# Performance work log

Measured on AMD Instinct MI355X. Metric: run time of the kernel, lower is better.

The kernel has to match this reference:

```python
import jax, jax.numpy as jnp
import numpy as np

EPS = 1e-12  # F.normalize default eps

def _l2norm(a, axis):
    n = jnp.sqrt(jnp.sum(a * a, axis=axis, keepdims=True))
    return a / jnp.maximum(n, EPS)

def setup_inputs() -> dict:
    key = jax.random.key(0)
    kx, kc = jax.random.split(key)
    x = jax.random.normal(kx, (32, 64, 64, 64), dtype=jnp.float32)        # [B,C,H,W]
    codebook = 0.2 * jax.random.normal(kc, (512, 64), dtype=jnp.float32)  # nn.init.normal_(w, 0, 0.2)
    return {"x": x, "codebook": codebook}

def reference(x, codebook):
    # mode == 'angular': normalize codebook rows and x along dim=1 (channels)
    cb = _l2norm(codebook, axis=1)          # [K,C]
    xn = _l2norm(x, axis=1)                 # [B,C,H,W]
    # x.transpose(-1, dim) with dim=1 -> swap axes 1 and 3
    xt = jnp.swapaxes(xn, 1, -1)            # [B,W,H,C]
    B, W, H, C = xt.shape
    flat = xt.reshape(-1, C)                # [N,C]
    d = (jnp.sum(cb * cb, axis=1)[None, :]
         + jnp.sum(flat * flat, axis=1, keepdims=True)
         - 2.0 * flat @ cb.T)               # [N,K]
    idx = jnp.argmin(d, axis=1)             # [N]
    codes = cb[idx].reshape(B, W, H, C)
    indices = idx.reshape(B, W, H)
    codes = jnp.swapaxes(codes, 1, -1)      # back to [B,C,H,W]
    indices = jnp.swapaxes(indices, 1, -1)  # [B,H,W]
    return codes, indices
```

## Files before the change

### kernel.cpp

```cpp
#include <hip/hip_runtime.h>

#define VQ_EPS    1e-12f
#define VQ_WINDOW 0.01f
#define VQ_CAP    12

typedef short bf16x8 __attribute__((ext_vector_type(8)));
typedef float f32x4  __attribute__((ext_vector_type(4)));

static __device__ __forceinline__ unsigned short f2bf(float f) {
    unsigned u = __float_as_uint(f);
    u += 0x7fffu + ((u >> 16) & 1u);
    return (unsigned short)(u >> 16);
}

static __device__ __forceinline__ unsigned f2ord(float f) {
    unsigned b = __float_as_uint(f);
    return (b & 0x80000000u) ? ~b : (b | 0x80000000u);
}

static __device__ __forceinline__ void wave_lds_fence() {
    asm volatile("s_waitcnt lgkmcnt(0)" ::: "memory");
}

__global__ __launch_bounds__(64) void cb_prep_kernel(const float* __restrict__ cb,
                                                     float* __restrict__ cbn,
                                                     unsigned short* __restrict__ cbB,
                                                     float* __restrict__ kn2,
                                                     float* __restrict__ kn2p) {
    const int k = blockIdx.x;
    const int c = threadIdx.x;
    float v = cb[k * 64 + c];
    float s = v * v;
    #pragma unroll
    for (int off = 32; off > 0; off >>= 1) s += __shfl_xor(s, off, 64);
    float n = sqrtf(s);
    float cn = v / fmaxf(n, VQ_EPS);
    cbn[k * 64 + c] = cn;

    const int ntile = k >> 4, col = k & 15;
    const int ks = c >> 5, quad = (c >> 3) & 3, j = c & 7;
    cbB[(((ntile * 2 + ks) * 64) + quad * 16 + col) * 8 + j] = f2bf(cn);

    float s2 = cn * cn;
    #pragma unroll
    for (int off = 32; off > 0; off >>= 1) s2 += __shfl_xor(s2, off, 64);
    if (c == 0) { kn2[k] = s2; kn2p[k] = s2 + 2.0f; }
}

__global__ __launch_bounds__(1024, 8) void vq_mfma_kernel(const float* __restrict__ x,
                                                      const float* __restrict__ cbn,
                                                      const unsigned short* __restrict__ cbB,
                                                      const float* __restrict__ kn2,
                                                      const float* __restrict__ kn2p,
                                                      float* __restrict__ codes,
                                                      float* __restrict__ idxout) {
    __shared__ __align__(16) unsigned short lcb[32768];
    __shared__ unsigned long long spack[256];
    __shared__ int slist[256][VQ_CAP];
    __shared__ int scnt[256];

    const int t    = threadIdx.x;
    const int lane = t & 63;
    const int wid  = t >> 6;
    const int col  = lane & 15;
    const int quad = lane >> 4;
    const int wr   = wid & 3;
    const int rsel = wid >> 2;
    const int wpix = wr * 16 + col;
    const int pbase = rsel * 64;
    const int pslot = pbase + wpix;

    const int rowid = blockIdx.x * 4 + rsel;
    const int b = rowid >> 6;
    const int h = rowid & 63;
    const float* xblk = x + ((size_t)b << 18) + (h << 6);

    if (quad == 0) { scnt[pslot] = 0; spack[pslot] = 0xFFFFFFFFFFFFFFFFull; }

    float xv[16];
    #pragma unroll
    for (int ks = 0; ks < 2; ++ks)
        #pragma unroll
        for (int j = 0; j < 8; ++j)
            xv[ks * 8 + j] = xblk[(size_t)(ks * 32 + quad * 8 + j) * 4096 + wpix];

    {
        const uint4* g4 = (const uint4*)cbB;
        uint4*       l4 = (uint4*)lcb;
        #pragma unroll
        for (int r = 0; r < 4; ++r) l4[r * 1024 + t] = g4[r * 1024 + t];
    }

    float ssp = 0.0f;
    #pragma unroll
    for (int i = 0; i < 16; ++i) ssp = fmaf(xv[i], xv[i], ssp);
    ssp += __shfl_xor(ssp, 16);
    ssp += __shfl_xor(ssp, 32);
    const float m2a = -2.0f * (1.0f / fmaxf(sqrtf(ssp), VQ_EPS));
    float m2r[4];
    #pragma unroll
    for (int r = 0; r < 4; ++r) m2r[r] = __shfl(m2a, quad * 4 + r);
    const float m2P = __shfl(m2a, lane >> 2);

    bf16x8 afrag[2];
    #pragma unroll
    for (int ks = 0; ks < 2; ++ks)
        #pragma unroll
        for (int j = 0; j < 8; ++j)
            ((unsigned short*)&afrag[ks])[j] = f2bf(xv[ks * 8 + j]);

    __syncthreads();

    const bf16x8* lBf = (const bf16x8*)lcb;

    unsigned run1[4] = {0xFFFFFFFFu, 0xFFFFFFFFu, 0xFFFFFFFFu, 0xFFFFFFFFu};
    unsigned run2[4] = {0xFFFFFFFFu, 0xFFFFFFFFu, 0xFFFFFFFFu, 0xFFFFFFFFu};
    #pragma unroll 4
    for (int nt = 0; nt < 32; ++nt) {
        bf16x8 b0 = lBf[(nt * 2 + 0) * 64 + lane];
        bf16x8 b1 = lBf[(nt * 2 + 1) * 64 + lane];
        f32x4 c = {0.0f, 0.0f, 0.0f, 0.0f};
        c = __builtin_amdgcn_mfma_f32_16x16x32_bf16(afrag[0], b0, c, 0, 0, 0);
        c = __builtin_amdgcn_mfma_f32_16x16x32_bf16(afrag[1], b1, c, 0, 0, 0);
        const float    kn   = kn2p[nt * 16 + col];
        const unsigned kidx = (unsigned)(nt * 16 + col);
        #pragma unroll
        for (int r = 0; r < 4; ++r) {
            float s = fmaf(m2r[r], c[r], kn);
            unsigned key = (__float_as_uint(s) & 0xFFFFFE00u) | kidx;
            unsigned mx  = max(run1[r], key);
            run1[r] = min(run1[r], key);
            run2[r] = min(run2[r], mx);
        }
    }

    float thr[4];
    #pragma unroll
    for (int r = 0; r < 4; ++r) {
        unsigned v = run1[r];
        v = min(v, (unsigned)__shfl_xor((int)v, 1));
        v = min(v, (unsigned)__shfl_xor((int)v, 2));
        v = min(v, (unsigned)__shfl_xor((int)v, 4));
        v = min(v, (unsigned)__shfl_xor((int)v, 8));
        thr[r] = __uint_as_float(v & 0xFFFFFE00u) + VQ_WINDOW;
    }

    bool f = false;
    #pragma unroll
    for (int r = 0; r < 4; ++r)
        f |= (__uint_as_float(run2[r] & 0xFFFFFE00u) <= thr[r]);
    const unsigned long long waveflag = __ballot(f);

    if (waveflag != 0ull) {
        #pragma unroll 4
        for (int nt = 0; nt < 32; ++nt) {
            bf16x8 b0 = lBf[(nt * 2 + 0) * 64 + lane];
            bf16x8 b1 = lBf[(nt * 2 + 1) * 64 + lane];
            f32x4 c = {0.0f, 0.0f, 0.0f, 0.0f};
            c = __builtin_amdgcn_mfma_f32_16x16x32_bf16(afrag[0], b0, c, 0, 0, 0);
            c = __builtin_amdgcn_mfma_f32_16x16x32_bf16(afrag[1], b1, c, 0, 0, 0);
            const float kn   = kn2p[nt * 16 + col];
            const int   kidx = nt * 16 + col;
            #pragma unroll
            for (int r = 0; r < 4; ++r) {
                float s = fmaf(m2r[r], c[r], kn);
                if (s <= thr[r]) {
                    int pix = pbase + wr * 16 + quad * 4 + r;
                    int pos = atomicAdd(&scnt[pix], 1);
                    if (pos < VQ_CAP) slist[pix][pos] = kidx;
                }
            }
        }
    } else {
        #pragma unroll
        for (int r = 0; r < 4; ++r) {
            float s1 = __uint_as_float(run1[r] & 0xFFFFFE00u);
            if (s1 <= thr[r]) {
                int pix = pbase + wr * 16 + quad * 4 + r;
                int pos = atomicAdd(&scnt[pix], 1);
                if (pos < VQ_CAP) slist[pix][pos] = (int)(run1[r] & 0x1FFu);
            }
        }
    }
    wave_lds_fence();

    {
        const int pw   = wr * 16 + (lane >> 2);
        const int P    = pbase + pw;
        const int sub  = lane & 3;
        const int cnt  = scnt[P];
        if (cnt > 1) {
            const float* xp = xblk + pw;
            if (cnt <= VQ_CAP) {
                for (int i = sub; i < cnt; i += 4) {
                    const int k = slist[P][i];
                    const float* cr = cbn + (size_t)k * 64;
                    float dot = 0.0f;
                    #pragma unroll 8
                    for (int c = 0; c < 64; ++c)
                        dot = fmaf(xp[(size_t)c * 4096], cr[c], dot);
                    float s = fmaf(m2P, dot, kn2[k]);
                    unsigned long long key =
                        ((unsigned long long)f2ord(s) << 32) | (unsigned)k;
                    atomicMin(&spack[P], key);
                }
            } else {
                for (int k = sub; k < 512; k += 4) {
                    const float* cr = cbn + (size_t)k * 64;
                    float dot = 0.0f;
                    #pragma unroll 8
                    for (int c = 0; c < 64; ++c)
                        dot = fmaf(xp[(size_t)c * 4096], cr[c], dot);
                    float s = fmaf(m2P, dot, kn2[k]);
                    unsigned long long key =
                        ((unsigned long long)f2ord(s) << 32) | (unsigned)k;
                    atomicMin(&spack[P], key);
                }
            }
        }
    }
    wave_lds_fence();

    const int cntw = scnt[pslot];
    const int bk = (cntw == 1) ? slist[pslot][0]
                               : (int)(spack[pslot] & 0xFFFFFFFFull);

    if (quad == 0) idxout[rowid * 64 + wpix] = (float)bk;

    {
        const float4* crow = (const float4*)(cbn + (size_t)bk * 64) + quad * 4;
        float* cp = codes + ((size_t)b << 18) + (h << 6) + wpix;
        #pragma unroll
        for (int q = 0; q < 4; ++q) {
            float4 v = crow[q];
            const int c0 = quad * 16 + q * 4;
            cp[(size_t)(c0 + 0) * 4096] = v.x;
            cp[(size_t)(c0 + 1) * 4096] = v.y;
            cp[(size_t)(c0 + 2) * 4096] = v.z;
            cp[(size_t)(c0 + 3) * 4096] = v.w;
        }
    }
}

extern "C" void kernel_launch(void* const* d_in, const int* in_sizes, int n_in,
                              void* d_out, int out_size, void* d_ws, size_t ws_size,
                              hipStream_t stream) {
    const float* x  = (const float*)d_in[0];
    const float* cb = (const float*)d_in[1];

    float*          cbn  = (float*)d_ws;
    unsigned short* cbB  = (unsigned short*)(cbn + 512 * 64);
    float*          kn2  = (float*)(cbB + 32768);
    float*          kn2p = kn2 + 512;

    float* codes  = (float*)d_out;
    float* idxout = codes + (size_t)32 * 64 * 64 * 64;

    cb_prep_kernel<<<512, 64, 0, stream>>>(cb, cbn, cbB, kn2, kn2p);
    vq_mfma_kernel<<<512, 1024, 0, stream>>>(x, cbn, cbB, kn2, kn2p, codes, idxout);
}
```

Measured before the change: 118.2 us.

## Halve block size and process two pixel rows per wave sequentially

```diff
diff --git a/kernel.cpp b/kernel.cpp
--- a/kernel.cpp
+++ b/kernel.cpp
@@ -47,7 +47,7 @@
     if (c == 0) { kn2[k] = s2; kn2p[k] = s2 + 2.0f; }
 }
 
-__global__ __launch_bounds__(1024, 8) void vq_mfma_kernel(const float* __restrict__ x,
+__global__ __launch_bounds__(512, 4) void vq_mfma_kernel(const float* __restrict__ x,
                                                       const float* __restrict__ cbn,
                                                       const unsigned short* __restrict__ cbB,
                                                       const float* __restrict__ kn2,
@@ -67,105 +67,120 @@
     const int wr   = wid & 3;
     const int rsel = wid >> 2;
     const int wpix = wr * 16 + col;
-    const int pbase = rsel * 64;
-    const int pslot = pbase + wpix;
-
-    const int rowid = blockIdx.x * 4 + rsel;
-    const int b = rowid >> 6;
-    const int h = rowid & 63;
-    const float* xblk = x + ((size_t)b << 18) + (h << 6);
-
-    if (quad == 0) { scnt[pslot] = 0; spack[pslot] = 0xFFFFFFFFFFFFFFFFull; }
-
-    float xv[16];
+
+    const int pbaseA = rsel * 64;
+    const int pbaseB = pbaseA + 128;
+    const int pslotA = pbaseA + wpix;
+    const int pslotB = pbaseB + wpix;
+
+    const int rowidA = blockIdx.x * 4 + rsel;
+    const int rowidB = rowidA + 2;
+    const int bA = rowidA >> 6, hA = rowidA & 63;
+    const int bB = rowidB >> 6, hB = rowidB & 63;
+    const float* xblkA = x + ((size_t)bA << 18) + (hA << 6);
+    const float* xblkB = x + ((size_t)bB << 18) + (hB << 6);
+
+    if (quad == 0) {
+        scnt[pslotA] = 0; spack[pslotA] = 0xFFFFFFFFFFFFFFFFull;
+        scnt[pslotB] = 0; spack[pslotB] = 0xFFFFFFFFFFFFFFFFull;
+    }
+
+    float xvA[16];
     #pragma unroll
     for (int ks = 0; ks < 2; ++ks)
         #pragma unroll
         for (int j = 0; j < 8; ++j)
-            xv[ks * 8 + j] = xblk[(size_t)(ks * 32 + quad * 8 + j) * 4096 + wpix];
+            xvA[ks * 8 + j] = xblkA[(size_t)(ks * 32 + quad * 8 + j) * 4096 + wpix];
 
     {
         const uint4* g4 = (const uint4*)cbB;
         uint4*       l4 = (uint4*)lcb;
         #pragma unroll
-        for (int r = 0; r < 4; ++r) l4[r * 1024 + t] = g4[r * 1024 + t];
-    }
-
-    float ssp = 0.0f;
-    #pragma unroll
-    for (int i = 0; i < 16; ++i) ssp = fmaf(xv[i], xv[i], ssp);
-    ssp += __shfl_xor(ssp, 16);
-    ssp += __shfl_xor(ssp, 32);
-    const float m2a = -2.0f * (1.0f / fmaxf(sqrtf(ssp), VQ_EPS));
-    float m2r[4];
-    #pragma unroll
-    for (int r = 0; r < 4; ++r) m2r[r] = __shfl(m2a, quad * 4 + r);
-    const float m2P = __shfl(m2a, lane >> 2);
-
-    bf16x8 afrag[2];
+        for (int r = 0; r < 8; ++r) l4[r * 512 + t] = g4[r * 512 + t];
+    }
+
+    __syncthreads();
+
+    float sspA = 0.0f;
+    #pragma unroll
+    for (int i = 0; i < 16; ++i) sspA = fmaf(xvA[i], xvA[i], sspA);
+    sspA += __shfl_xor(sspA, 16);
+    sspA += __shfl_xor(sspA, 32);
+    const float m2aA = -2.0f * (1.0f / fmaxf(sqrtf(sspA), VQ_EPS));
+    float m2rA[4];
+    #pragma unroll
+    for (int r = 0; r < 4; ++r) m2rA[r] = __shfl(m2aA, quad * 4 + r);
+    const float m2PA = __shfl(m2aA, lane >> 2);
+
+    bf16x8 afragA[2];
     #pragma unroll
     for (int ks = 0; ks < 2; ++ks)
         #pragma unroll
         for (int j = 0; j < 8; ++j)
-            ((unsigned short*)&afrag[ks])[j] = f2bf(xv[ks * 8 + j]);
-
-    __syncthreads();
+            ((unsigned short*)&afragA[ks])[j] = f2bf(xvA[ks * 8 + j]);
+
+    float xvB[16];
+    #pragma unroll
+    for (int ks = 0; ks < 2; ++ks)
+        #pragma unroll
+        for (int j = 0; j < 8; ++j)
+            xvB[ks * 8 + j] = xblkB[(size_t)(ks * 32 + quad * 8 + j) * 4096 + wpix];
 
     const bf16x8* lBf = (const bf16x8*)lcb;
 
-    unsigned run1[4] = {0xFFFFFFFFu, 0xFFFFFFFFu, 0xFFFFFFFFu, 0xFFFFFFFFu};
-    unsigned run2[4] = {0xFFFFFFFFu, 0xFFFFFFFFu, 0xFFFFFFFFu, 0xFFFFFFFFu};
+    unsigned run1A[4] = {0xFFFFFFFFu, 0xFFFFFFFFu, 0xFFFFFFFFu, 0xFFFFFFFFu};
+    unsigned run2A[4] = {0xFFFFFFFFu, 0xFFFFFFFFu, 0xFFFFFFFFu, 0xFFFFFFFFu};
     #pragma unroll 4
     for (int nt = 0; nt < 32; ++nt) {
         bf16x8 b0 = lBf[(nt * 2 + 0) * 64 + lane];
         bf16x8 b1 = lBf[(nt * 2 + 1) * 64 + lane];
         f32x4 c = {0.0f, 0.0f, 0.0f, 0.0f};
-        c = __builtin_amdgcn_mfma_f32_16x16x32_bf16(afrag[0], b0, c, 0, 0, 0);
-        c = __builtin_amdgcn_mfma_f32_16x16x32_bf16(afrag[1], b1, c, 0, 0, 0);
+        c = __builtin_amdgcn_mfma_f32_16x16x32_bf16(afragA[0], b0, c, 0, 0, 0);
+        c = __builtin_amdgcn_mfma_f32_16x16x32_bf16(afragA[1], b1, c, 0, 0, 0);
         const float    kn   = kn2p[nt * 16 + col];
         const unsigned kidx = (unsigned)(nt * 16 + col);
         #pragma unroll
         for (int r = 0; r < 4; ++r) {
-            float s = fmaf(m2r[r], c[r], kn);
+            float s = fmaf(m2rA[r], c[r], kn);
             unsigned key = (__float_as_uint(s) & 0xFFFFFE00u) | kidx;
-            unsigned mx  = max(run1[r], key);
-            run1[r] = min(run1[r], key);
-            run2[r] = min(run2[r], mx);
-        }
-    }
-
-    float thr[4];
+            unsigned mx  = max(run1A[r], key);
+            run1A[r] = min(run1A[r], key);
+            run2A[r] = min(run2A[r], mx);
+        }
+    }
+
+    float thrA[4];
     #pragma unroll
     for (int r = 0; r < 4; ++r) {
-        unsigned v = run1[r];
+        unsigned v = run1A[r];
         v = min(v, (unsigned)__shfl_xor((int)v, 1));
         v = min(v, (unsigned)__shfl_xor((int)v, 2));
         v = min(v, (unsigned)__shfl_xor((int)v, 4));
         v = min(v, (unsigned)__shfl_xor((int)v, 8));
-        thr[r] = __uint_as_float(v & 0xFFFFFE00u) + VQ_WINDOW;
-    }
-
-    bool f = false;
+        thrA[r] = __uint_as_float(v & 0xFFFFFE00u) + VQ_WINDOW;
+    }
+
+    bool fA = false;
     #pragma unroll
     for (int r = 0; r < 4; ++r)
-        f |= (__uint_as_float(run2[r] & 0xFFFFFE00u) <= thr[r]);
-    const unsigned long long waveflag = __ballot(f);
-
-    if (waveflag != 0ull) {
+        fA |= (__uint_as_float(run2A[r] & 0xFFFFFE00u) <= thrA[r]);
+    const unsigned long long waveflagA = __ballot(fA);
+
+    if (waveflagA != 0ull) {
         #pragma unroll 4
         for (int nt = 0; nt < 32; ++nt) {
             bf16x8 b0 = lBf[(nt * 2 + 0) * 64 + lane];
             bf16x8 b1 = lBf[(nt * 2 + 1) * 64 + lane];
             f32x4 c = {0.0f, 0.0f, 0.0f, 0.0f};
-            c = __builtin_amdgcn_mfma_f32_16x16x32_bf16(afrag[0], b0, c, 0, 0, 0);
-            c = __builtin_amdgcn_mfma_f32_16x16x32_bf16(afrag[1], b1, c, 0, 0, 0);
+            c = __builtin_amdgcn_mfma_f32_16x16x32_bf16(afragA[0], b0, c, 0, 0, 0);
+            c = __builtin_amdgcn_mfma_f32_16x16x32_bf16(afragA[1], b1, c, 0, 0, 0);
             const float kn   = kn2p[nt * 16 + col];
             const int   kidx = nt * 16 + col;
             #pragma unroll
             for (int r = 0; r < 4; ++r) {
-                float s = fmaf(m2r[r], c[r], kn);
-                if (s <= thr[r]) {
-                    int pix = pbase + wr * 16 + quad * 4 + r;
+                float s = fmaf(m2rA[r], c[r], kn);
+                if (s <= thrA[r]) {
+                    int pix = pbaseA + wr * 16 + quad * 4 + r;
                     int pos = atomicAdd(&scnt[pix], 1);
                     if (pos < VQ_CAP) slist[pix][pos] = kidx;
                 }
@@ -174,23 +189,41 @@
     } else {
         #pragma unroll
         for (int r = 0; r < 4; ++r) {
-            float s1 = __uint_as_float(run1[r] & 0xFFFFFE00u);
-            if (s1 <= thr[r]) {
-                int pix = pbase + wr * 16 + quad * 4 + r;
+            float s1 = __uint_as_float(run1A[r] & 0xFFFFFE00u);
+            if (s1 <= thrA[r]) {
+                int pix = pbaseA + wr * 16 + quad * 4 + r;
                 int pos = atomicAdd(&scnt[pix], 1);
-                if (pos < VQ_CAP) slist[pix][pos] = (int)(run1[r] & 0x1FFu);
+                if (pos < VQ_CAP) slist[pix][pos] = (int)(run1A[r] & 0x1FFu);
             }
         }
     }
     wave_lds_fence();
 
+    float sspB = 0.0f;
+    #pragma unroll
+    for (int i = 0; i < 16; ++i) sspB = fmaf(xvB[i], xvB[i], sspB);
+    sspB += __shfl_xor(sspB, 16);
+    sspB += __shfl_xor(sspB, 32);
+    const float m2aB = -2.0f * (1.0f / fmaxf(sqrtf(sspB), VQ_EPS));
+    float m2rB[4];
+    #pragma unroll
+    for (int r = 0; r < 4; ++r) m2rB[r] = __shfl(m2aB, quad * 4 + r);
+    const float m2PB = __shfl(m2aB, lane >> 2);
+
+    bf16x8 afragB[2];
+    #pragma unroll
+    for (int ks = 0; ks < 2; ++ks)
+        #pragma unroll
+        for (int j = 0; j < 8; ++j)
+            ((unsigned short*)&afragB[ks])[j] = f2bf(xvB[ks * 8 + j]);
+
     {
-        const int pw   = wr * 16 + (lane >> 2);
-        const int P    = pbase + pw;
-        const int sub  = lane & 3;
-        const int cnt  = scnt[P];
+        const int pw  = wr * 16 + (lane >> 2);
+        const int P   = pbaseA + pw;
+        const int sub = lane & 3;
+        const int cnt = scnt[P];
         if (cnt > 1) {
-            const float* xp = xblk + pw;
+            const float* xp = xblkA + pw;
             if (cnt <= VQ_CAP) {
                 for (int i = sub; i < cnt; i += 4) {
                     const int k = slist[P][i];
@@ -199,7 +232,7 @@
                     #pragma unroll 8
                     for (int c = 0; c < 64; ++c)
                         dot = fmaf(xp[(size_t)c * 4096], cr[c], dot);
-                    float s = fmaf(m2P, dot, kn2[k]);
+                    float s = fmaf(m2PA, dot, kn2[k]);
                     unsigned long long key =
                         ((unsigned long long)f2ord(s) << 32) | (unsigned)k;
                     atomicMin(&spack[P], key);
@@ -211,7 +244,7 @@
                     #pragma unroll 8
                     for (int c = 0; c < 64; ++c)
                         dot = fmaf(xp[(size_t)c * 4096], cr[c], dot);
-                    float s = fmaf(m2P, dot, kn2[k]);
+                    float s = fmaf(m2PA, dot, kn2[k]);
                     unsigned long long key =
                         ((unsigned long long)f2ord(s) << 32) | (unsigned)k;
                     atomicMin(&spack[P], key);
@@ -221,15 +254,13 @@
     }
     wave_lds_fence();
 
-    const int cntw = scnt[pslot];
-    const int bk = (cntw == 1) ? slist[pslot][0]
-                               : (int)(spack[pslot] & 0xFFFFFFFFull);
-
-    if (quad == 0) idxout[rowid * 64 + wpix] = (float)bk;
-
     {
+        const int cntw = scnt[pslotA];
+        const int bk = (cntw == 1) ? slist[pslotA][0]
+                                   : (int)(spack[pslotA] & 0xFFFFFFFFull);
+        if (quad == 0) idxout[rowidA * 64 + wpix] = (float)bk;
         const float4* crow = (const float4*)(cbn + (size_t)bk * 64) + quad * 4;
-        float* cp = codes + ((size_t)b << 18) + (h << 6) + wpix;
+        float* cp = codes + ((size_t)bA << 18) + (hA << 6) + wpix;
         #pragma unroll
         for (int q = 0; q < 4; ++q) {
             float4 v = crow[q];
@@ -240,6 +271,132 @@
             cp[(size_t)(c0 + 3) * 4096] = v.w;
         }
     }
+
+    unsigned run1B[4] = {0xFFFFFFFFu, 0xFFFFFFFFu, 0xFFFFFFFFu, 0xFFFFFFFFu};
+    unsigned run2B[4] = {0xFFFFFFFFu, 0xFFFFFFFFu, 0xFFFFFFFFu, 0xFFFFFFFFu};
+    #pragma unroll 4
+    for (int nt = 0; nt < 32; ++nt) {
+        bf16x8 b0 = lBf[(nt * 2 + 0) * 64 + lane];
+        bf16x8 b1 = lBf[(nt * 2 + 1) * 64 + lane];
+        f32x4 c = {0.0f, 0.0f, 0.0f, 0.0f};
+        c = __builtin_amdgcn_mfma_f32_16x16x32_bf16(afragB[0], b0, c, 0, 0, 0);
+        c = __builtin_amdgcn_mfma_f32_16x16x32_bf16(afragB[1], b1, c, 0, 0, 0);
+        const float    kn   = kn2p[nt * 16 + col];
+        const unsigned kidx = (unsigned)(nt * 16 + col);
+        #pragma unroll
+        for (int r = 0; r < 4; ++r) {
+            float s = fmaf(m2rB[r], c[r], kn);
+            unsigned key = (__float_as_uint(s) & 0xFFFFFE00u) | kidx;
+            unsigned mx  = max(run1B[r], key);
+            run1B[r] = min(run1B[r], key);
+            run2B[r] = min(run2B[r], mx);
+        }
+    }
+
+    float thrB[4];
+    #pragma unroll
+    for (int r = 0; r < 4; ++r) {
+        unsigned v = run1B[r];
+        v = min(v, (unsigned)__shfl_xor((int)v, 1));
+        v = min(v, (unsigned)__shfl_xor((int)v, 2));
+        v = min(v, (unsigned)__shfl_xor((int)v, 4));
+        v = min(v, (unsigned)__shfl_xor((int)v, 8));
+        thrB[r] = __uint_as_float(v & 0xFFFFFE00u) + VQ_WINDOW;
+    }
+
+    bool fB = false;
+    #pragma unroll
+    for (int r = 0; r < 4; ++r)
+        fB |= (__uint_as_float(run2B[r] & 0xFFFFFE00u) <= thrB[r]);
+    const unsigned long long waveflagB = __ballot(fB);
+
+    if (waveflagB != 0ull) {
+        #pragma unroll 4
+        for (int nt = 0; nt < 32; ++nt) {
+            bf16x8 b0 = lBf[(nt * 2 + 0) * 64 + lane];
+            bf16x8 b1 = lBf[(nt * 2 + 1) * 64 + lane];
+            f32x4 c = {0.0f, 0.0f, 0.0f, 0.0f};
+            c = __builtin_amdgcn_mfma_f32_16x16x32_bf16(afragB[0], b0, c, 0, 0, 0);
+            c = __builtin_amdgcn_mfma_f32_16x16x32_bf16(afragB[1], b1, c, 0, 0, 0);
+            const float kn   = kn2p[nt * 16 + col];
+            const int   kidx = nt * 16 + col;
+            #pragma unroll
+            for (int r = 0; r < 4; ++r) {
+                float s = fmaf(m2rB[r], c[r], kn);
+                if (s <= thrB[r]) {
+                    int pix = pbaseB + wr * 16 + quad * 4 + r;
+                    int pos = atomicAdd(&scnt[pix], 1);
+                    if (pos < VQ_CAP) slist[pix][pos] = kidx;
+                }
+            }
+        }
+    } else {
+        #pragma unroll
+        for (int r = 0; r < 4; ++r) {
+            float s1 = __uint_as_float(run1B[r] & 0xFFFFFE00u);
+            if (s1 <= thrB[r]) {
+                int pix = pbaseB + wr * 16 + quad * 4 + r;
+                int pos = atomicAdd(&scnt[pix], 1);
+                if (pos < VQ_CAP) slist[pix][pos] = (int)(run1B[r] & 0x1FFu);
+            }
+        }
+    }
+    wave_lds_fence();
+
+    {
+        const int pw  = wr * 16 + (lane >> 2);
+        const int P   = pbaseB + pw;
+        const int sub = lane & 3;
+        const int cnt = scnt[P];
+        if (cnt > 1) {
+            const float* xp = xblkB + pw;
+            if (cnt <= VQ_CAP) {
+                for (int i = sub; i < cnt; i += 4) {
+                    const int k = slist[P][i];
+                    const float* cr = cbn + (size_t)k * 64;
+                    float dot = 0.0f;
+                    #pragma unroll 8
+                    for (int c = 0; c < 64; ++c)
+                        dot = fmaf(xp[(size_t)c * 4096], cr[c], dot);
+                    float s = fmaf(m2PB, dot, kn2[k]);
+                    unsigned long long key =
+                        ((unsigned long long)f2ord(s) << 32) | (unsigned)k;
+                    atomicMin(&spack[P], key);
+                }
+            } else {
+                for (int k = sub; k < 512; k += 4) {
+                    const float* cr = cbn + (size_t)k * 64;
+                    float dot = 0.0f;
+                    #pragma unroll 8
+                    for (int c = 0; c < 64; ++c)
+                        dot = fmaf(xp[(size_t)c * 4096], cr[c], dot);
+                    float s = fmaf(m2PB, dot, kn2[k]);
+                    unsigned long long key =
+                        ((unsigned long long)f2ord(s) << 32) | (unsigned)k;
+                    atomicMin(&spack[P], key);
+                }
+            }
+        }
+    }
+    wave_lds_fence();
+
+    {
+        const int cntw = scnt[pslotB];
+        const int bk = (cntw == 1) ? slist[pslotB][0]
+                                   : (int)(spack[pslotB] & 0xFFFFFFFFull);
+        if (quad == 0) idxout[rowidB * 64 + wpix] = (float)bk;
+        const float4* crow = (const float4*)(cbn + (size_t)bk * 64) + quad * 4;
+        float* cp = codes + ((size_t)bB << 18) + (hB << 6) + wpix;
+        #pragma unroll
+        for (int q = 0; q < 4; ++q) {
+            float4 v = crow[q];
+            const int c0 = quad * 16 + q * 4;
+            cp[(size_t)(c0 + 0) * 4096] = v.x;
+            cp[(size_t)(c0 + 1) * 4096] = v.y;
+            cp[(size_t)(c0 + 2) * 4096] = v.z;
+            cp[(size_t)(c0 + 3) * 4096] = v.w;
+        }
+    }
 }
 
 extern "C" void kernel_launch(void* const* d_in, const int* in_sizes, int n_in,
@@ -257,5 +414,5 @@
     float* idxout = codes + (size_t)32 * 64 * 64 * 64;
 
     cb_prep_kernel<<<512, 64, 0, stream>>>(cb, cbn, cbB, kn2, kn2p);
-    vq_mfma_kernel<<<512, 1024, 0, stream>>>(x, cbn, cbB, kn2, kn2p, codes, idxout);
-}
+    vq_mfma_kernel<<<512, 512, 0, stream>>>(x, cbn, cbB, kn2, kn2p, codes, idxout);
+}
```

New measurement: 123.9 us. 4.9% more time.

## Process two image rows per wave to reuse codebook fragments across MFMAs

Applied to the files above, without the earlier changes.

```diff
diff --git a/kernel.cpp b/kernel.cpp
--- a/kernel.cpp
+++ b/kernel.cpp
@@ -47,7 +47,7 @@
     if (c == 0) { kn2[k] = s2; kn2p[k] = s2 + 2.0f; }
 }
 
-__global__ __launch_bounds__(1024, 8) void vq_mfma_kernel(const float* __restrict__ x,
+__global__ __launch_bounds__(512, 4) void vq_mfma_kernel(const float* __restrict__ x,
                                                       const float* __restrict__ cbn,
                                                       const unsigned short* __restrict__ cbB,
                                                       const float* __restrict__ kn2,
@@ -65,171 +65,262 @@
     const int col  = lane & 15;
     const int quad = lane >> 4;
     const int wr   = wid & 3;
-    const int rsel = wid >> 2;
+    const int grp  = wid >> 2;
     const int wpix = wr * 16 + col;
-    const int pbase = rsel * 64;
-    const int pslot = pbase + wpix;
-
-    const int rowid = blockIdx.x * 4 + rsel;
-    const int b = rowid >> 6;
-    const int h = rowid & 63;
-    const float* xblk = x + ((size_t)b << 18) + (h << 6);
-
-    if (quad == 0) { scnt[pslot] = 0; spack[pslot] = 0xFFFFFFFFFFFFFFFFull; }
-
-    float xv[16];
+
+    const int rw0 = grp * 2;
+    const int rw1 = rw0 + 1;
+    const int pbase0 = rw0 * 64;
+    const int pbase1 = rw1 * 64;
+    const int pslot0 = pbase0 + wpix;
+    const int pslot1 = pbase1 + wpix;
+
+    const int rowid0 = blockIdx.x * 4 + rw0;
+    const int rowid1 = rowid0 + 1;
+    const int b0r = rowid0 >> 6, h0 = rowid0 & 63;
+    const int b1r = rowid1 >> 6, h1 = rowid1 & 63;
+    const float* xblk0 = x + ((size_t)b0r << 18) + (h0 << 6);
+    const float* xblk1 = x + ((size_t)b1r << 18) + (h1 << 6);
+
+    if (quad == 0) {
+        scnt[pslot0] = 0; spack[pslot0] = 0xFFFFFFFFFFFFFFFFull;
+        scnt[pslot1] = 0; spack[pslot1] = 0xFFFFFFFFFFFFFFFFull;
+    }
+
+    float xv0[16], xv1[16];
     #pragma unroll
     for (int ks = 0; ks < 2; ++ks)
         #pragma unroll
         for (int j = 0; j < 8; ++j)
-            xv[ks * 8 + j] = xblk[(size_t)(ks * 32 + quad * 8 + j) * 4096 + wpix];
+            xv0[ks * 8 + j] = xblk0[(size_t)(ks * 32 + quad * 8 + j) * 4096 + wpix];
+    #pragma unroll
+    for (int ks = 0; ks < 2; ++ks)
+        #pragma unroll
+        for (int j = 0; j < 8; ++j)
+            xv1[ks * 8 + j] = xblk1[(size_t)(ks * 32 + quad * 8 + j) * 4096 + wpix];
 
     {
         const uint4* g4 = (const uint4*)cbB;
         uint4*       l4 = (uint4*)lcb;
         #pragma unroll
-        for (int r = 0; r < 4; ++r) l4[r * 1024 + t] = g4[r * 1024 + t];
-    }
-
-    float ssp = 0.0f;
-    #pragma unroll
-    for (int i = 0; i < 16; ++i) ssp = fmaf(xv[i], xv[i], ssp);
-    ssp += __shfl_xor(ssp, 16);
-    ssp += __shfl_xor(ssp, 32);
-    const float m2a = -2.0f * (1.0f / fmaxf(sqrtf(ssp), VQ_EPS));
-    float m2r[4];
-    #pragma unroll
-    for (int r = 0; r < 4; ++r) m2r[r] = __shfl(m2a, quad * 4 + r);
-    const float m2P = __shfl(m2a, lane >> 2);
-
-    bf16x8 afrag[2];
+        for (int r = 0; r < 8; ++r) l4[r * 512 + t] = g4[r * 512 + t];
+    }
+
+    __syncthreads();
+
+    float ssp0 = 0.0f, ssp1 = 0.0f;
+    #pragma unroll
+    for (int i = 0; i < 16; ++i) ssp0 = fmaf(xv0[i], xv0[i], ssp0);
+    #pragma unroll
+    for (int i = 0; i < 16; ++i) ssp1 = fmaf(xv1[i], xv1[i], ssp1);
+    ssp0 += __shfl_xor(ssp0, 16);
+    ssp0 += __shfl_xor(ssp0, 32);
+    ssp1 += __shfl_xor(ssp1, 16);
+    ssp1 += __shfl_xor(ssp1, 32);
+    const float m2a0 = -2.0f * (1.0f / fmaxf(sqrtf(ssp0), VQ_EPS));
+    const float m2a1 = -2.0f * (1.0f / fmaxf(sqrtf(ssp1), VQ_EPS));
+    float m2r0[4], m2r1[4];
+    #pragma unroll
+    for (int r = 0; r < 4; ++r) m2r0[r] = __shfl(m2a0, quad * 4 + r);
+    #pragma unroll
+    for (int r = 0; r < 4; ++r) m2r1[r] = __shfl(m2a1, quad * 4 + r);
+    const float m2P0 = __shfl(m2a0, lane >> 2);
+    const float m2P1 = __shfl(m2a1, lane >> 2);
+
+    bf16x8 afrag0[2], afrag1[2];
     #pragma unroll
     for (int ks = 0; ks < 2; ++ks)
         #pragma unroll
-        for (int j = 0; j < 8; ++j)
-            ((unsigned short*)&afrag[ks])[j] = f2bf(xv[ks * 8 + j]);
-
-    __syncthreads();
+        for (int j = 0; j < 8; ++j) {
+            ((unsigned short*)&afrag0[ks])[j] = f2bf(xv0[ks * 8 + j]);
+            ((unsigned short*)&afrag1[ks])[j] = f2bf(xv1[ks * 8 + j]);
+        }
 
     const bf16x8* lBf = (const bf16x8*)lcb;
 
-    unsigned run1[4] = {0xFFFFFFFFu, 0xFFFFFFFFu, 0xFFFFFFFFu, 0xFFFFFFFFu};
-    unsigned run2[4] = {0xFFFFFFFFu, 0xFFFFFFFFu, 0xFFFFFFFFu, 0xFFFFFFFFu};
-    #pragma unroll 4
+    unsigned run1_0[4] = {0xFFFFFFFFu, 0xFFFFFFFFu, 0xFFFFFFFFu, 0xFFFFFFFFu};
+    unsigned run2_0[4] = {0xFFFFFFFFu, 0xFFFFFFFFu, 0xFFFFFFFFu, 0xFFFFFFFFu};
+    unsigned run1_1[4] = {0xFFFFFFFFu, 0xFFFFFFFFu, 0xFFFFFFFFu, 0xFFFFFFFFu};
+    unsigned run2_1[4] = {0xFFFFFFFFu, 0xFFFFFFFFu, 0xFFFFFFFFu, 0xFFFFFFFFu};
+    #pragma unroll 2
     for (int nt = 0; nt < 32; ++nt) {
         bf16x8 b0 = lBf[(nt * 2 + 0) * 64 + lane];
         bf16x8 b1 = lBf[(nt * 2 + 1) * 64 + lane];
-        f32x4 c = {0.0f, 0.0f, 0.0f, 0.0f};
-        c = __builtin_amdgcn_mfma_f32_16x16x32_bf16(afrag[0], b0, c, 0, 0, 0);
-        c = __builtin_amdgcn_mfma_f32_16x16x32_bf16(afrag[1], b1, c, 0, 0, 0);
+        f32x4 c0 = {0.0f, 0.0f, 0.0f, 0.0f};
+        f32x4 c1 = {0.0f, 0.0f, 0.0f, 0.0f};
+        c0 = __builtin_amdgcn_mfma_f32_16x16x32_bf16(afrag0[0], b0, c0, 0, 0, 0);
+        c1 = __builtin_amdgcn_mfma_f32_16x16x32_bf16(afrag1[0], b0, c1, 0, 0, 0);
+        c0 = __builtin_amdgcn_mfma_f32_16x16x32_bf16(afrag0[1], b1, c0, 0, 0, 0);
+        c1 = __builtin_amdgcn_mfma_f32_16x16x32_bf16(afrag1[1], b1, c1, 0, 0, 0);
         const float    kn   = kn2p[nt * 16 + col];
         const unsigned kidx = (unsigned)(nt * 16 + col);
         #pragma unroll
         for (int r = 0; r < 4; ++r) {
-            float s = fmaf(m2r[r], c[r], kn);
-            unsigned key = (__float_as_uint(s) & 0xFFFFFE00u) | kidx;
-            unsigned mx  = max(run1[r], key);
-            run1[r] = min(run1[r], key);
-            run2[r] = min(run2[r], mx);
-        }
-    }
-
-    float thr[4];
+            float s0 = fmaf(m2r0[r], c0[r], kn);
+            unsigned key0 = (__float_as_uint(s0) & 0xFFFFFE00u) | kidx;
+            unsigned mx0  = max(run1_0[r], key0);
+            run1_0[r] = min(run1_0[r], key0);
+            run2_0[r] = min(run2_0[r], mx0);
+            float s1 = fmaf(m2r1[r], c1[r], kn);
+            unsigned key1 = (__float_as_uint(s1) & 0xFFFFFE00u) | kidx;
+            unsigned mx1  = max(run1_1[r], key1);
+            run1_1[r] = min(run1_1[r], key1);
+            run2_1[r] = min(run2_1[r], mx1);
+        }
+    }
+
+    float thr0[4], thr1[4];
     #pragma unroll
     for (int r = 0; r < 4; ++r) {
-        unsigned v = run1[r];
+        unsigned v = run1_0[r];
         v = min(v, (unsigned)__shfl_xor((int)v, 1));
         v = min(v, (unsigned)__shfl_xor((int)v, 2));
         v = min(v, (unsigned)__shfl_xor((int)v, 4));
         v = min(v, (unsigned)__shfl_xor((int)v, 8));
-        thr[r] = __uint_as_float(v & 0xFFFFFE00u) + VQ_WINDOW;
+        thr0[r] = __uint_as_float(v & 0xFFFFFE00u) + VQ_WINDOW;
+        unsigned w = run1_1[r];
+        w = min(w, (unsigned)__shfl_xor((int)w, 1));
+        w = min(w, (unsigned)__shfl_xor((int)w, 2));
+        w = min(w, (unsigned)__shfl_xor((int)w, 4));
+        w = min(w, (unsigned)__shfl_xor((int)w, 8));
+        thr1[r] = __uint_as_float(w & 0xFFFFFE00u) + VQ_WINDOW;
     }
 
     bool f = false;
     #pragma unroll
-    for (int r = 0; r < 4; ++r)
-        f |= (__uint_as_float(run2[r] & 0xFFFFFE00u) <= thr[r]);
+    for (int r = 0; r < 4; ++r) {
+        f |= (__uint_as_float(run2_0[r] & 0xFFFFFE00u) <= thr0[r]);
+        f |= (__uint_as_float(run2_1[r] & 0xFFFFFE00u) <= thr1[r]);
+    }
     const unsigned long long waveflag = __ballot(f);
 
     if (waveflag != 0ull) {
-        #pragma unroll 4
+        #pragma unroll 2
         for (int nt = 0; nt < 32; ++nt) {
             bf16x8 b0 = lBf[(nt * 2 + 0) * 64 + lane];
             bf16x8 b1 = lBf[(nt * 2 + 1) * 64 + lane];
-            f32x4 c = {0.0f, 0.0f, 0.0f, 0.0f};
-            c = __builtin_amdgcn_mfma_f32_16x16x32_bf16(afrag[0], b0, c, 0, 0, 0);
-            c = __builtin_amdgcn_mfma_f32_16x16x32_bf16(afrag[1], b1, c, 0, 0, 0);
+            f32x4 c0 = {0.0f, 0.0f, 0.0f, 0.0f};
+            f32x4 c1 = {0.0f, 0.0f, 0.0f, 0.0f};
+            c0 = __builtin_amdgcn_mfma_f32_16x16x32_bf16(afrag0[0], b0, c0, 0, 0, 0);
+            c1 = __builtin_amdgcn_mfma_f32_16x16x32_bf16(afrag1[0], b0, c1, 0, 0, 0);
+            c0 = __builtin_amdgcn_mfma_f32_16x16x32_bf16(afrag0[1], b1, c0, 0, 0, 0);
+            c1 = __builtin_amdgcn_mfma_f32_16x16x32_bf16(afrag1[1], b1, c1, 0, 0, 0);
             const float kn   = kn2p[nt * 16 + col];
             const int   kidx = nt * 16 + col;
             #pragma unroll
             for (int r = 0; r < 4; ++r) {
-                float s = fmaf(m2r[r], c[r], kn);
-                if (s <= thr[r]) {
-                    int pix = pbase + wr * 16 + quad * 4 + r;
+                float s0 = fmaf(m2r0[r], c0[r], kn);
+                if (s0 <= thr0[r]) {
+                    int pix = pbase0 + wr * 16 + quad * 4 + r;
                     int pos = atomicAdd(&scnt[pix], 1);
                     if (pos < VQ_CAP) slist[pix][pos] = kidx;
                 }
+                float s1 = fmaf(m2r1[r], c1[r], kn);
+                if (s1 <= thr1[r]) {
+                    int pix = pbase1 + wr * 16 + quad * 4 + r;
+                    int pos = atomicAdd(&scnt[pix], 1);
+                    if (pos < VQ_CAP) slist[pix][pos] = kidx;
+                }
             }
         }
     } else {
         #pragma unroll
         for (int r = 0; r < 4; ++r) {
-            float s1 = __uint_as_float(run1[r] & 0xFFFFFE00u);
-            if (s1 <= thr[r]) {
-                int pix = pbase + wr * 16 + quad * 4 + r;
+            float s0 = __uint_as_float(run1_0[r] & 0xFFFFFE00u);
+            if (s0 <= thr0[r]) {
+                int pix = pbase0 + wr * 16 + quad * 4 + r;
                 int pos = atomicAdd(&scnt[pix], 1);
-                if (pos < VQ_CAP) slist[pix][pos] = (int)(run1[r] & 0x1FFu);
+                if (pos < VQ_CAP) slist[pix][pos] = (int)(run1_0[r] & 0x1FFu);
+            }
+            float s1 = __uint_as_float(run1_1[r] & 0xFFFFFE00u);
+            if (s1 <= thr1[r]) {
+                int pix = pbase1 + wr * 16 + quad * 4 + r;
+                int pos = atomicAdd(&scnt[pix], 1);
+                if (pos < VQ_CAP) slist[pix][pos] = (int)(run1_1[r] & 0x1FFu);
             }
         }
     }
     wave_lds_fence();
 
     {
-        const int pw   = wr * 16 + (lane >> 2);
-        const int P    = pbase + pw;
-        const int sub  = lane & 3;
-        const int cnt  = scnt[P];
-        if (cnt > 1) {
-            const float* xp = xblk + pw;
-            if (cnt <= VQ_CAP) {
-                for (int i = sub; i < cnt; i += 4) {
-                    const int k = slist[P][i];
-                    const float* cr = cbn + (size_t)k * 64;
-                    float dot = 0.0f;
-                    #pragma unroll 8
-                    for (int c = 0; c < 64; ++c)
-                        dot = fmaf(xp[(size_t)c * 4096], cr[c], dot);
-                    float s = fmaf(m2P, dot, kn2[k]);
-                    unsigned long long key =
-                        ((unsigned long long)f2ord(s) << 32) | (unsigned)k;
-                    atomicMin(&spack[P], key);
+        const int pw  = wr * 16 + (lane >> 2);
+        const int sub = lane & 3;
+        {
+            const int P   = pbase0 + pw;
+            const int cnt = scnt[P];
+            if (cnt > 1) {
+                const float* xp = xblk0 + pw;
+                if (cnt <= VQ_CAP) {
+                    for (int i = sub; i < cnt; i += 4) {
+                        const int k = slist[P][i];
+                        const float* cr = cbn + (size_t)k * 64;
+                        float dot = 0.0f;
+                        #pragma unroll 8
+                        for (int c = 0; c < 64; ++c)
+                            dot = fmaf(xp[(size_t)c * 4096], cr[c], dot);
+                        float s = fmaf(m2P0, dot, kn2[k]);
+                        unsigned long long key =
+                            ((unsigned long long)f2ord(s) << 32) | (unsigned)k;
+                        atomicMin(&spack[P], key);
+                    }
+                } else {
+                    for (int k = sub; k < 512; k += 4) {
+                        const float* cr = cbn + (size_t)k * 64;
+                        float dot = 0.0f;
+                        #pragma unroll 8
+                        for (int c = 0; c < 64; ++c)
+                            dot = fmaf(xp[(size_t)c * 4096], cr[c], dot);
+                        float s = fmaf(m2P0, dot, kn2[k]);
+                        unsigned long long key =
+                            ((unsigned long long)f2ord(s) << 32) | (unsigned)k;
+                        atomicMin(&spack[P], key);
+                    }
                 }
-            } else {
-                for (int k = sub; k < 512; k += 4) {
-                    const float* cr = cbn + (size_t)k * 64;
-                    float dot = 0.0f;
-                    #pragma unroll 8
-                    for (int c = 0; c < 64; ++c)
-                        dot = fmaf(xp[(size_t)c * 4096], cr[c], dot);
-                    float s = fmaf(m2P, dot, kn2[k]);
-                    unsigned long long key =
-                        ((unsigned long long)f2ord(s) << 32) | (unsigned)k;
-                    atomicMin(&spack[P], key);
+            }
+        }
+        {
+            const int P   = pbase1 + pw;
+            const int cnt = scnt[P];
+            if (cnt > 1) {
+                const float* xp = xblk1 + pw;
+                if (cnt <= VQ_CAP) {
+                    for (int i = sub; i < cnt; i += 4) {
+                        const int k = slist[P][i];
+                        const float* cr = cbn + (size_t)k * 64;
+                        float dot = 0.0f;
+                        #pragma unroll 8
+                        for (int c = 0; c < 64; ++c)
+                            dot = fmaf(xp[(size_t)c * 4096], cr[c], dot);
+                        float s = fmaf(m2P1, dot, kn2[k]);
+                        unsigned long long key =
+                            ((unsigned long long)f2ord(s) << 32) | (unsigned)k;
+                        atomicMin(&spack[P], key);
+                    }
+                } else {
+                    for (int k = sub; k < 512; k += 4) {
+                        const float* cr = cbn + (size_t)k * 64;
+                        float dot = 0.0f;
+                        #pragma unroll 8
+                        for (int c = 0; c < 64; ++c)
+                            dot = fmaf(xp[(size_t)c * 4096], cr[c], dot);
+                        float s = fmaf(m2P1, dot, kn2[k]);
+                        unsigned long long key =
+                            ((unsigned long long)f2ord(s) << 32) | (unsigned)k;
+                        atomicMin(&spack[P], key);
+                    }
                 }
             }
         }
     }
     wave_lds_fence();
 
-    const int cntw = scnt[pslot];
-    const int bk = (cntw == 1) ? slist[pslot][0]
-                               : (int)(spack[pslot] & 0xFFFFFFFFull);
-
-    if (quad == 0) idxout[rowid * 64 + wpix] = (float)bk;
-
     {
+        const int cntw = scnt[pslot0];
+        const int bk = (cntw == 1) ? slist[pslot0][0]
+                                   : (int)(spack[pslot0] & 0xFFFFFFFFull);
+        if (quad == 0) idxout[rowid0 * 64 + wpix] = (float)bk;
         const float4* crow = (const float4*)(cbn + (size_t)bk * 64) + quad * 4;
-        float* cp = codes + ((size_t)b << 18) + (h << 6) + wpix;
+        float* cp = codes + ((size_t)b0r << 18) + (h0 << 6) + wpix;
         #pragma unroll
         for (int q = 0; q < 4; ++q) {
             float4 v = crow[q];
@@ -240,6 +331,23 @@
             cp[(size_t)(c0 + 3) * 4096] = v.w;
         }
     }
+    {
+        const int cntw = scnt[pslot1];
+        const int bk = (cntw == 1) ? slist[pslot1][0]
+                                   : (int)(spack[pslot1] & 0xFFFFFFFFull);
+        if (quad == 0) idxout[rowid1 * 64 + wpix] = (float)bk;
+        const float4* crow = (const float4*)(cbn + (size_t)bk * 64) + quad * 4;
+        float* cp = codes + ((size_t)b1r << 18) + (h1 << 6) + wpix;
+        #pragma unroll
+        for (int q = 0; q < 4; ++q) {
+            float4 v = crow[q];
+            const int c0 = quad * 16 + q * 4;
+            cp[(size_t)(c0 + 0) * 4096] = v.x;
+            cp[(size_t)(c0 + 1) * 4096] = v.y;
+            cp[(size_t)(c0 + 2) * 4096] = v.z;
+            cp[(size_t)(c0 + 3) * 4096] = v.w;
+        }
+    }
 }
 
 extern "C" void kernel_launch(void* const* d_in, const int* in_sizes, int n_in,
@@ -257,5 +365,5 @@
     float* idxout = codes + (size_t)32 * 64 * 64 * 64;
 
     cb_prep_kernel<<<512, 64, 0, stream>>>(cb, cbn, cbB, kn2, kn2p);
-    vq_mfma_kernel<<<512, 1024, 0, stream>>>(x, cbn, cbB, kn2, kn2p, codes, idxout);
-}
+    vq_mfma_kernel<<<512, 512, 0, stream>>>(x, cbn, cbB, kn2, kn2p, codes, idxout);
+}
```

After: 122.8 us. 3.9% more time.
